# Kernel optimization log

Measured on AMD Instinct MI355X. Metric: run time of the kernel, lower is better.

Reference implementation:

```python
import jax, jax.numpy as jnp
import numpy as np

N_NODES = 50000
N_EDGES = 800000
HIDDEN = 64
RES = 0.5  # args.res_layer


def setup_inputs() -> dict:
    key = jax.random.key(0)
    ks = jax.random.split(key, 9)
    s = 0.05  # scale weights to keep exp(att) stable
    return {
        "edge_index": jax.random.randint(ks[0], (2, N_EDGES), 0, N_NODES, dtype=jnp.int32),
        "adj_values": jax.random.uniform(ks[1], (N_EDGES,), dtype=jnp.float32),
        "embeds": jax.random.normal(ks[2], (N_NODES, HIDDEN), dtype=jnp.float32),
        "W1": jax.random.normal(ks[3], (HIDDEN, HIDDEN), dtype=jnp.float32) * s,
        "b1": jax.random.normal(ks[4], (HIDDEN,), dtype=jnp.float32) * s,
        "W2": jax.random.normal(ks[5], (HIDDEN, HIDDEN), dtype=jnp.float32) * s,
        "b2": jax.random.normal(ks[6], (HIDDEN,), dtype=jnp.float32) * s,
        "att_w": jax.random.normal(ks[7], (2 * HIDDEN,), dtype=jnp.float32) * s,
        "att_b": jax.random.normal(ks[8], (1,), dtype=jnp.float32) * s,
    }


def reference(edge_index, adj_values, embeds, W1, b1, W2, b2, att_w, att_b):
    n = embeds.shape[0]
    h = embeds.shape[1]
    row, col = edge_index[0], edge_index[1]
    # per-edge gather + two small linears with ReLU
    f1 = jax.nn.relu(embeds[row] @ W1 + b1)          # [E, h]
    f2 = jax.nn.relu(embeds[col] @ W2 + b2)          # [E, h]
    # attention score = Linear(concat(f1, f2)) -> split weight, avoid concat
    att = f1 @ att_w[:h] + f2 @ att_w[h:] + att_b[0]  # [E]
    exp_att = jnp.exp(att)
    # sparse row-wise softmax denominator via segment sum
    rowsum = jax.ops.segment_sum(exp_att, row, num_segments=n) + 1e-6  # [N]
    values = (exp_att / rowsum[row] + RES * adj_values) / (1.0 + RES)  # [E]
    # SpMM: out[i] = sum_{e: row[e]=i} values[e] * embeds[col[e]]
    out = jax.ops.segment_sum(values[:, None] * embeds[col], row, num_segments=n)  # [N, h]
    return values, out
```

## Files before the change

kernel.cpp:

```cpp
#include <hip/hip_runtime.h>
#include <hip/hip_bf16.h>

#define HID 64
#define RES_F 0.5f
#define NBKT 196
#define BCAP 5120
#define EB   256
#define LCAP 48

typedef __attribute__((ext_vector_type(8))) short short8;
typedef __attribute__((ext_vector_type(4))) float f32x4;

__device__ __forceinline__ float lane_bcast_f(float v, int k) {
    return __builtin_bit_cast(float, __builtin_amdgcn_readlane(__builtin_bit_cast(int, v), k));
}
__device__ __forceinline__ short f2bf(float x) {
    __hip_bfloat16 h = __float2bfloat16(x);
    return __builtin_bit_cast(short, h);
}
__device__ __forceinline__ float bf2f(unsigned short u) {
    return __builtin_bit_cast(float, ((unsigned)u) << 16);
}

__global__ void __launch_bounds__(256) fused_prep_kernel(
    const float* __restrict__ embeds,
    const float* __restrict__ W1, const float* __restrict__ W2,
    const float* __restrict__ b1, const float* __restrict__ b2,
    const float* __restrict__ att_w, const float* __restrict__ att_b,
    const int* __restrict__ row, const int* __restrict__ col,
    const float* __restrict__ adj,
    int2* __restrict__ bstream, int* __restrict__ bcnt,
    float* __restrict__ g, float* __restrict__ corr,
    __hip_bfloat16* __restrict__ embeds_bf,
    int n, int E, int nodeBlocks)
{
    __shared__ short sW[2 * HID * HID];

    if (blockIdx.x < nodeBlocks) {
        for (int i = threadIdx.x; i < HID * HID; i += blockDim.x) {
            sW[i]             = f2bf(W1[i]);
            sW[HID * HID + i] = f2bf(W2[i]);
        }
        __syncthreads();

        const float ab = att_b[0];
        const int lane = threadIdx.x & 63;
        const int colx = lane & 15;
        const int quad = lane >> 4;

        short8 bfrag[8][2];
        float  sac[8], bc[8];
#pragma unroll
        for (int cb = 0; cb < 8; ++cb) {
            const int jp = cb * 16 + colx;
            const short* w = (jp < HID) ? (sW + jp) : (sW + HID * HID + jp - HID);
#pragma unroll
            for (int kh = 0; kh < 2; ++kh) {
                short8 f;
#pragma unroll
                for (int j = 0; j < 8; ++j) {
                    const int k = kh * 32 + quad * 8 + j;
                    f[j] = w[k * HID];
                }
                bfrag[cb][kh] = f;
            }
            sac[cb] = att_w[jp];
            bc[cb]  = (jp < HID) ? b1[jp] : b2[jp - HID];
        }

        int gwave = (blockIdx.x * blockDim.x + threadIdx.x) >> 6;
        const int nwave = (nodeBlocks * blockDim.x) >> 6;
        const int nbatch = (n + 15) >> 4;

        for (int b = gwave; b < nbatch; b += nwave) {
            const int base = b << 4;
            int mrow = base + colx;
            if (mrow >= n) mrow = n - 1;
            const float* ep = embeds + (size_t)mrow * HID;
            short8 afrag0, afrag1;
#pragma unroll
            for (int j = 0; j < 8; ++j) {
                afrag0[j] = f2bf(ep[quad * 8 + j]);
                afrag1[j] = f2bf(ep[32 + quad * 8 + j]);
            }
            {
                short8* ebf = (short8*)(embeds_bf + (size_t)mrow * HID);
                ebf[quad]     = afrag0;
                ebf[4 + quad] = afrag1;
            }

            float acc1[4] = {0.f, 0.f, 0.f, 0.f};
            float acc2[4] = {0.f, 0.f, 0.f, 0.f};
#pragma unroll
            for (int cb = 0; cb < 8; ++cb) {
                f32x4 C = {0.f, 0.f, 0.f, 0.f};
                C = __builtin_amdgcn_mfma_f32_16x16x32_bf16(afrag0, bfrag[cb][0], C, 0, 0, 0);
                C = __builtin_amdgcn_mfma_f32_16x16x32_bf16(afrag1, bfrag[cb][1], C, 0, 0, 0);
#pragma unroll
                for (int reg = 0; reg < 4; ++reg) {
                    const float v = fmaxf(C[reg] + bc[cb], 0.f) * sac[cb];
                    if (cb < 4) acc1[reg] += v; else acc2[reg] += v;
                }
            }
#pragma unroll
            for (int reg = 0; reg < 4; ++reg) {
#pragma unroll
                for (int off = 1; off < 16; off <<= 1) {
                    acc1[reg] += __shfl_xor(acc1[reg], off, 64);
                    acc2[reg] += __shfl_xor(acc2[reg], off, 64);
                }
            }
            if (colx == 0) {
#pragma unroll
                for (int reg = 0; reg < 4; ++reg) {
                    const int i = base + quad * 4 + reg;
                    if (i < n) {
                        g[i]    = __expf(acc2[reg]);
                        corr[i] = 1e-6f * __expf(-(acc1[reg] + ab));
                    }
                }
            }
        }
    } else {
        int* lcnt = (int*)sW;
        for (int k = threadIdx.x; k < NBKT; k += 256) lcnt[k] = 0;
        __syncthreads();

        const int eb = blockIdx.x - nodeBlocks;
        const int chunk = (E + EB - 1) / EB;
        const int e0 = eb * chunk;
        const int e1 = min(E, e0 + chunk);
        for (int e = e0 + (int)threadIdx.x; e < e1; e += 256) {
            const int r    = row[e];
            const int c    = col[e];
            const float aj = adj[e];
            const unsigned aq = (unsigned)(aj * 65535.0f + 0.5f);
            const int k = r >> 8;
            const int2 pl = make_int2((int)((unsigned)c | (aq << 16)),
                                      (r & 255) | (e << 8));
            const int pos = atomicAdd(&lcnt[k], 1);
            if (pos < LCAP)
                bstream[((size_t)k * EB + eb) * LCAP + pos] = pl;
        }
        __syncthreads();

        for (int k = threadIdx.x; k < NBKT; k += 256)
            bcnt[eb * NBKT + k] = min(lcnt[k], LCAP);
    }
}

__global__ void __launch_bounds__(256) regroup_kernel(
    const int2* __restrict__ bstream, const int* __restrict__ bcnt,
    int2* __restrict__ edata2, int* __restrict__ rowdir, int n)
{
    __shared__ int cnt[256], scan[256], wcur[256];
    const int k = blockIdx.x;
    const int t = threadIdx.x;
    cnt[t] = 0;
    const int myc = bcnt[t * NBKT + k];
    __syncthreads();

    const int2* src = bstream + ((size_t)k * EB + t) * LCAP;
    for (int j = 0; j < myc; ++j)
        atomicAdd(&cnt[src[j].y & 255], 1);
    __syncthreads();

    scan[t] = cnt[t];
    __syncthreads();
    for (int ofs = 1; ofs < 256; ofs <<= 1) {
        const int v = (t >= ofs) ? scan[t - ofs] : 0;
        __syncthreads();
        scan[t] += v;
        __syncthreads();
    }
    const int excl = scan[t] - cnt[t];
    wcur[t] = excl;
    const int r = k * 256 + t;
    if (r < n)
        rowdir[r] = (k * BCAP + excl) | (min(cnt[t], 64) << 20);
    __syncthreads();

    int2* dst = edata2 + (size_t)k * BCAP;
    for (int j = 0; j < myc; ++j) {
        const int2 pl = src[j];
        const int p = atomicAdd(&wcur[pl.y & 255], 1);
        dst[p] = pl;
    }
}

__global__ void __launch_bounds__(256) spmm_kernel(
    const int* __restrict__ rowdir, const int2* __restrict__ edata2,
    const __hip_bfloat16* __restrict__ embeds_bf,
    const float* __restrict__ g, const float* __restrict__ corr,
    float* __restrict__ values, float* __restrict__ out, int n)
{
    const float inv = 1.0f / (1.0f + RES_F);
    const int lane = threadIdx.x & 63;
    const int half = lane >> 5;
    const int hl   = lane & 31;
    int r = (blockIdx.x * blockDim.x + threadIdx.x) >> 6;
    const int nwave = (gridDim.x * blockDim.x) >> 6;

    for (; r < n; r += nwave) {
        const int pk    = rowdir[r];
        const int start = pk & 0xFFFFF;
        const int deg   = pk >> 20;
        const bool valid = lane < deg;
        int c = 0, e = 0;
        float gc = 0.0f, aj = 0.0f;
        if (valid) {
            const int2 ed = edata2[(size_t)start + lane];
            const unsigned pk0 = (unsigned)ed.x;
            c  = (int)(pk0 & 0xFFFFu);
            aj = (float)(pk0 >> 16) * (1.0f / 65535.0f);
            e  = (int)(((unsigned)ed.y) >> 8);
            gc = g[c];
        }
        float G = gc;
#pragma unroll
        for (int off = 1; off < 64; off <<= 1)
            G += __shfl_xor(G, off, 64);
        const float invDr = 1.0f / (G + corr[r]);
        float v = 0.0f;
        if (valid) {
            v = (gc * invDr + RES_F * aj) * inv;
            values[e] = v;
        }

        float accx = 0.0f, accy = 0.0f;
        int j = 0;
        for (; j + 8 <= deg; j += 8) {
            const int j0 = j + half,     j1 = j + 2 + half;
            const int j2 = j + 4 + half, j3 = j + 6 + half;
            const int   c0 = __shfl(c, j0, 64);
            const int   c1 = __shfl(c, j1, 64);
            const int   c2 = __shfl(c, j2, 64);
            const int   c3 = __shfl(c, j3, 64);
            const float v0 = __shfl(v, j0, 64);
            const float v1 = __shfl(v, j1, 64);
            const float v2 = __shfl(v, j2, 64);
            const float v3 = __shfl(v, j3, 64);
            const ushort2 h0 = *(const ushort2*)(embeds_bf + (size_t)c0 * HID + hl * 2);
            const ushort2 h1 = *(const ushort2*)(embeds_bf + (size_t)c1 * HID + hl * 2);
            const ushort2 h2 = *(const ushort2*)(embeds_bf + (size_t)c2 * HID + hl * 2);
            const ushort2 h3 = *(const ushort2*)(embeds_bf + (size_t)c3 * HID + hl * 2);
            accx = fmaf(v0, bf2f(h0.x), accx); accy = fmaf(v0, bf2f(h0.y), accy);
            accx = fmaf(v1, bf2f(h1.x), accx); accy = fmaf(v1, bf2f(h1.y), accy);
            accx = fmaf(v2, bf2f(h2.x), accx); accy = fmaf(v2, bf2f(h2.y), accy);
            accx = fmaf(v3, bf2f(h3.x), accx); accy = fmaf(v3, bf2f(h3.y), accy);
        }
        for (; j < deg; j += 2) {
            const int j0 = j + half;
            const int   cj = __shfl(c, j0, 64);
            const float vj = __shfl(v, j0, 64);
            const ushort2 h = *(const ushort2*)(embeds_bf + (size_t)cj * HID + hl * 2);
            accx = fmaf(vj, bf2f(h.x), accx);
            accy = fmaf(vj, bf2f(h.y), accy);
        }
        accx += __shfl_xor(accx, 32, 64);
        accy += __shfl_xor(accy, 32, 64);
        if (lane < 32) {
            float2 o; o.x = accx; o.y = accy;
            ((float2*)(out + (size_t)r * HID))[hl] = o;
        }
    }
}

extern "C" void kernel_launch(void* const* d_in, const int* in_sizes, int n_in,
                              void* d_out, int out_size, void* d_ws, size_t ws_size,
                              hipStream_t stream_)
{
    const int* edge_index = (const int*)d_in[0];
    const float* adj      = (const float*)d_in[1];
    const float* embeds   = (const float*)d_in[2];
    const float* W1       = (const float*)d_in[3];
    const float* b1       = (const float*)d_in[4];
    const float* W2       = (const float*)d_in[5];
    const float* b2       = (const float*)d_in[6];
    const float* att_w    = (const float*)d_in[7];
    const float* att_b    = (const float*)d_in[8];

    const int E = in_sizes[1];
    const int N = in_sizes[2] / HID;

    const int* row = edge_index;
    const int* col = edge_index + E;

    int2*  bstream = (int2*)d_ws;
    int2*  edata2  = bstream + (size_t)NBKT * EB * LCAP;
    int*   bcnt    = (int*)(edata2 + (size_t)NBKT * BCAP);
    int*   rowdir  = bcnt + EB * NBKT;
    float* g       = (float*)(rowdir + N);
    float* corr    = g + N;
    __hip_bfloat16* embeds_bf = (__hip_bfloat16*)(corr + N);

    float* values = (float*)d_out;
    float* out    = values + E;

    const int nodeBlocks = 512;
    fused_prep_kernel<<<nodeBlocks + EB, 256, 0, stream_>>>(
        embeds, W1, W2, b1, b2, att_w, att_b, row, col, adj,
        bstream, bcnt, g, corr, embeds_bf,
        N, E, nodeBlocks);

    regroup_kernel<<<NBKT, 256, 0, stream_>>>(bstream, bcnt, edata2, rowdir, N);

    spmm_kernel<<<12544, 256, 0, stream_>>>(rowdir, edata2, embeds_bf,
                                            g, corr, values, out, N);
}
```

Before: 144.5 us.

## Move softmax normalization into regroup and write values in a coalesced pass

The per-row denominator is now accumulated with shared-memory float atomics during regroup, and final edge values are computed there and stored in edata2 in place of the packed adj and edge id. The SpMM kernel no longer does a wave reduction, gathers g, or scatters to values[e]. A new elementwise kernel writes values coalesced in edge order using an invD array. Regroup runs 512 threads per block, splits each bucket's edges between two halves, and uses a wave-shuffle scan instead of the barrier-heavy scan. The trade-offs are an extra launch, extra g/invD gathers, and a denominator summed in atomic order.

```diff
diff --git a/kernel.cpp b/kernel.cpp
--- a/kernel.cpp
+++ b/kernel.cpp
@@ -11,9 +11,6 @@
 typedef __attribute__((ext_vector_type(8))) short short8;
 typedef __attribute__((ext_vector_type(4))) float f32x4;
 
-__device__ __forceinline__ float lane_bcast_f(float v, int k) {
-    return __builtin_bit_cast(float, __builtin_amdgcn_readlane(__builtin_bit_cast(int, v), k));
-}
 __device__ __forceinline__ short f2bf(float x) {
     __hip_bfloat16 h = __float2bfloat16(x);
     return __builtin_bit_cast(short, h);
@@ -149,52 +146,86 @@
     }
 }
 
-__global__ void __launch_bounds__(256) regroup_kernel(
+__global__ void __launch_bounds__(512) regroup_kernel(
     const int2* __restrict__ bstream, const int* __restrict__ bcnt,
-    int2* __restrict__ edata2, int* __restrict__ rowdir, int n)
-{
-    __shared__ int cnt[256], scan[256], wcur[256];
-    const int k = blockIdx.x;
-    const int t = threadIdx.x;
-    cnt[t] = 0;
-    const int myc = bcnt[t * NBKT + k];
+    const float* __restrict__ g, const float* __restrict__ corr,
+    int2* __restrict__ edata2, int* __restrict__ rowdir,
+    float* __restrict__ invD, int n)
+{
+    __shared__ int   cnt[256], wcur[256], wsum[4];
+    __shared__ float Dsum[256];
+    const int k  = blockIdx.x;
+    const int t  = threadIdx.x;
+    const int sl = t & 255;
+    const bool hi = t >= 256;
+
+    if (!hi) {
+        cnt[sl] = 0;
+        const int r = k * 256 + sl;
+        Dsum[sl] = (r < n) ? corr[r] : 1.0f;
+    }
+    const int myc = bcnt[sl * NBKT + k];
+    const int jm  = (myc + 1) >> 1;
+    const int j0  = hi ? jm : 0;
+    const int j1  = hi ? myc : jm;
     __syncthreads();
 
-    const int2* src = bstream + ((size_t)k * EB + t) * LCAP;
-    for (int j = 0; j < myc; ++j)
-        atomicAdd(&cnt[src[j].y & 255], 1);
+    const int2* src = bstream + ((size_t)k * EB + sl) * LCAP;
+    for (int j = j0; j < j1; ++j) {
+        const int2 pl = src[j];
+        const int rloc = pl.y & 255;
+        atomicAdd(&cnt[rloc], 1);
+        atomicAdd(&Dsum[rloc], g[pl.x & 0xFFFF]);
+    }
     __syncthreads();
 
-    scan[t] = cnt[t];
+    int incl = 0, myCnt = 0;
+    if (!hi) {
+        const int lane = t & 63;
+        myCnt = cnt[t];
+        incl = myCnt;
+#pragma unroll
+        for (int off = 1; off < 64; off <<= 1) {
+            const int y = __shfl_up(incl, off, 64);
+            if (lane >= off) incl += y;
+        }
+        if (lane == 63) wsum[t >> 6] = incl;
+    }
     __syncthreads();
-    for (int ofs = 1; ofs < 256; ofs <<= 1) {
-        const int v = (t >= ofs) ? scan[t - ofs] : 0;
-        __syncthreads();
-        scan[t] += v;
-        __syncthreads();
-    }
-    const int excl = scan[t] - cnt[t];
-    wcur[t] = excl;
-    const int r = k * 256 + t;
-    if (r < n)
-        rowdir[r] = (k * BCAP + excl) | (min(cnt[t], 64) << 20);
+    if (!hi) {
+        const int w = t >> 6;
+        int wo = 0;
+        for (int i = 0; i < w; ++i) wo += wsum[i];
+        const int excl = incl + wo - myCnt;
+        wcur[t] = excl;
+        const float iD = 1.0f / Dsum[t];
+        const int r = k * 256 + t;
+        if (r < n) {
+            rowdir[r] = (k * BCAP + excl) | (min(myCnt, 64) << 20);
+            invD[r]   = iD;
+        }
+        Dsum[t] = iD;
+    }
     __syncthreads();
 
+    const float inv = 1.0f / (1.0f + RES_F);
     int2* dst = edata2 + (size_t)k * BCAP;
-    for (int j = 0; j < myc; ++j) {
+    for (int j = j0; j < j1; ++j) {
         const int2 pl = src[j];
-        const int p = atomicAdd(&wcur[pl.y & 255], 1);
-        dst[p] = pl;
+        const int rloc = pl.y & 255;
+        const int c    = pl.x & 0xFFFF;
+        const float aj = (float)((unsigned)pl.x >> 16) * (1.0f / 65535.0f);
+        const float v  = (g[c] * Dsum[rloc] + RES_F * aj) * inv;
+        const int p = atomicAdd(&wcur[rloc], 1);
+        dst[p] = make_int2(c, __float_as_int(v));
     }
 }
 
 __global__ void __launch_bounds__(256) spmm_kernel(
     const int* __restrict__ rowdir, const int2* __restrict__ edata2,
     const __hip_bfloat16* __restrict__ embeds_bf,
-    const float* __restrict__ g, const float* __restrict__ corr,
-    float* __restrict__ values, float* __restrict__ out, int n)
-{
-    const float inv = 1.0f / (1.0f + RES_F);
+    float* __restrict__ out, int n)
+{
     const int lane = threadIdx.x & 63;
     const int half = lane >> 5;
     const int hl   = lane & 31;
@@ -205,26 +236,12 @@
         const int pk    = rowdir[r];
         const int start = pk & 0xFFFFF;
         const int deg   = pk >> 20;
-        const bool valid = lane < deg;
-        int c = 0, e = 0;
-        float gc = 0.0f, aj = 0.0f;
-        if (valid) {
+        int c = 0;
+        float v = 0.0f;
+        if (lane < deg) {
             const int2 ed = edata2[(size_t)start + lane];
-            const unsigned pk0 = (unsigned)ed.x;
-            c  = (int)(pk0 & 0xFFFFu);
-            aj = (float)(pk0 >> 16) * (1.0f / 65535.0f);
-            e  = (int)(((unsigned)ed.y) >> 8);
-            gc = g[c];
-        }
-        float G = gc;
-#pragma unroll
-        for (int off = 1; off < 64; off <<= 1)
-            G += __shfl_xor(G, off, 64);
-        const float invDr = 1.0f / (G + corr[r]);
-        float v = 0.0f;
-        if (valid) {
-            v = (gc * invDr + RES_F * aj) * inv;
-            values[e] = v;
+            c = ed.x;
+            v = __int_as_float(ed.y);
         }
 
         float accx = 0.0f, accy = 0.0f;
@@ -266,6 +283,19 @@
     }
 }
 
+__global__ void __launch_bounds__(256) values_kernel(
+    const int* __restrict__ row, const int* __restrict__ col,
+    const float* __restrict__ adj,
+    const float* __restrict__ g, const float* __restrict__ invD,
+    float* __restrict__ values, int E)
+{
+    const int e = blockIdx.x * blockDim.x + threadIdx.x;
+    if (e < E) {
+        const float inv = 1.0f / (1.0f + RES_F);
+        values[e] = (g[col[e]] * invD[row[e]] + RES_F * adj[e]) * inv;
+    }
+}
+
 extern "C" void kernel_launch(void* const* d_in, const int* in_sizes, int n_in,
                               void* d_out, int out_size, void* d_ws, size_t ws_size,
                               hipStream_t stream_)
@@ -292,7 +322,8 @@
     int*   rowdir  = bcnt + EB * NBKT;
     float* g       = (float*)(rowdir + N);
     float* corr    = g + N;
-    __hip_bfloat16* embeds_bf = (__hip_bfloat16*)(corr + N);
+    float* invD    = corr + N;
+    __hip_bfloat16* embeds_bf = (__hip_bfloat16*)(invD + N);
 
     float* values = (float*)d_out;
     float* out    = values + E;
@@ -303,8 +334,12 @@
         bstream, bcnt, g, corr, embeds_bf,
         N, E, nodeBlocks);
 
-    regroup_kernel<<<NBKT, 256, 0, stream_>>>(bstream, bcnt, edata2, rowdir, N);
+    regroup_kernel<<<NBKT, 512, 0, stream_>>>(bstream, bcnt, g, corr,
+                                              edata2, rowdir, invD, N);
 
     spmm_kernel<<<12544, 256, 0, stream_>>>(rowdir, edata2, embeds_bf,
-                                            g, corr, values, out, N);
-}
+                                            out, N);
+
+    values_kernel<<<(E + 255) / 256, 256, 0, stream_>>>(row, col, adj, g,
+                                                        invD, values, E);
+}
```

Measured after the change: 147.5 us. 1.02x slower.

## Split regroup across 512 threads with wave-shuffle scan and remap spmm rows to waves

Applied to the files above, without the earlier changes.

The regroup kernel now runs 512 threads per bucket, each half handling half of every bucket sub-stream. The 256-entry block scan, which needed log-many barriers, becomes a wave-level shuffle scan plus a small cross-wave sum. The spmm kernel drops its grid-stride loop and assigns one row per wave with a block index permutation, so the 8 blocks sharing an index mod 8 cover interleaved buckets. This is meant to cut serial latency in regroup and spread edata2 and rowdir accesses across buckets, at the cost of more launched blocks and some early-exiting waves.

```diff
diff --git a/kernel.cpp b/kernel.cpp
--- a/kernel.cpp
+++ b/kernel.cpp
@@ -11,9 +11,6 @@
 typedef __attribute__((ext_vector_type(8))) short short8;
 typedef __attribute__((ext_vector_type(4))) float f32x4;
 
-__device__ __forceinline__ float lane_bcast_f(float v, int k) {
-    return __builtin_bit_cast(float, __builtin_amdgcn_readlane(__builtin_bit_cast(int, v), k));
-}
 __device__ __forceinline__ short f2bf(float x) {
     __hip_bfloat16 h = __float2bfloat16(x);
     return __builtin_bit_cast(short, h);
@@ -149,39 +146,54 @@
     }
 }
 
-__global__ void __launch_bounds__(256) regroup_kernel(
+__global__ void __launch_bounds__(512) regroup_kernel(
     const int2* __restrict__ bstream, const int* __restrict__ bcnt,
     int2* __restrict__ edata2, int* __restrict__ rowdir, int n)
 {
-    __shared__ int cnt[256], scan[256], wcur[256];
-    const int k = blockIdx.x;
-    const int t = threadIdx.x;
-    cnt[t] = 0;
-    const int myc = bcnt[t * NBKT + k];
+    __shared__ int cnt[256], wcur[256], wsum[4];
+    const int k  = blockIdx.x;
+    const int t  = threadIdx.x;
+    const int sl = t & 255;
+    const bool hi = t >= 256;
+
+    if (!hi) cnt[sl] = 0;
+    const int myc = bcnt[sl * NBKT + k];
+    const int jm  = (myc + 1) >> 1;
+    const int j0  = hi ? jm : 0;
+    const int j1  = hi ? myc : jm;
     __syncthreads();
 
-    const int2* src = bstream + ((size_t)k * EB + t) * LCAP;
-    for (int j = 0; j < myc; ++j)
+    const int2* src = bstream + ((size_t)k * EB + sl) * LCAP;
+    for (int j = j0; j < j1; ++j)
         atomicAdd(&cnt[src[j].y & 255], 1);
     __syncthreads();
 
-    scan[t] = cnt[t];
+    int incl = 0, myCnt = 0;
+    if (!hi) {
+        const int lane = t & 63;
+        myCnt = cnt[t];
+        incl = myCnt;
+#pragma unroll
+        for (int off = 1; off < 64; off <<= 1) {
+            const int y = __shfl_up(incl, off, 64);
+            if (lane >= off) incl += y;
+        }
+        if (lane == 63) wsum[t >> 6] = incl;
+    }
     __syncthreads();
-    for (int ofs = 1; ofs < 256; ofs <<= 1) {
-        const int v = (t >= ofs) ? scan[t - ofs] : 0;
-        __syncthreads();
-        scan[t] += v;
-        __syncthreads();
-    }
-    const int excl = scan[t] - cnt[t];
-    wcur[t] = excl;
-    const int r = k * 256 + t;
-    if (r < n)
-        rowdir[r] = (k * BCAP + excl) | (min(cnt[t], 64) << 20);
+    if (!hi) {
+        int wo = 0;
+        for (int i = 0; i < (t >> 6); ++i) wo += wsum[i];
+        const int excl = incl + wo - myCnt;
+        wcur[t] = excl;
+        const int r = k * 256 + t;
+        if (r < n)
+            rowdir[r] = (k * BCAP + excl) | (min(myCnt, 64) << 20);
+    }
     __syncthreads();
 
     int2* dst = edata2 + (size_t)k * BCAP;
-    for (int j = 0; j < myc; ++j) {
+    for (int j = j0; j < j1; ++j) {
         const int2 pl = src[j];
         const int p = atomicAdd(&wcur[pl.y & 255], 1);
         dst[p] = pl;
@@ -198,71 +210,72 @@
     const int lane = threadIdx.x & 63;
     const int half = lane >> 5;
     const int hl   = lane & 31;
-    int r = (blockIdx.x * blockDim.x + threadIdx.x) >> 6;
-    const int nwave = (gridDim.x * blockDim.x) >> 6;
-
-    for (; r < n; r += nwave) {
-        const int pk    = rowdir[r];
-        const int start = pk & 0xFFFFF;
-        const int deg   = pk >> 20;
-        const bool valid = lane < deg;
-        int c = 0, e = 0;
-        float gc = 0.0f, aj = 0.0f;
-        if (valid) {
-            const int2 ed = edata2[(size_t)start + lane];
-            const unsigned pk0 = (unsigned)ed.x;
-            c  = (int)(pk0 & 0xFFFFu);
-            aj = (float)(pk0 >> 16) * (1.0f / 65535.0f);
-            e  = (int)(((unsigned)ed.y) >> 8);
-            gc = g[c];
-        }
-        float G = gc;
-#pragma unroll
-        for (int off = 1; off < 64; off <<= 1)
-            G += __shfl_xor(G, off, 64);
-        const float invDr = 1.0f / (G + corr[r]);
-        float v = 0.0f;
-        if (valid) {
-            v = (gc * invDr + RES_F * aj) * inv;
-            values[e] = v;
-        }
-
-        float accx = 0.0f, accy = 0.0f;
-        int j = 0;
-        for (; j + 8 <= deg; j += 8) {
-            const int j0 = j + half,     j1 = j + 2 + half;
-            const int j2 = j + 4 + half, j3 = j + 6 + half;
-            const int   c0 = __shfl(c, j0, 64);
-            const int   c1 = __shfl(c, j1, 64);
-            const int   c2 = __shfl(c, j2, 64);
-            const int   c3 = __shfl(c, j3, 64);
-            const float v0 = __shfl(v, j0, 64);
-            const float v1 = __shfl(v, j1, 64);
-            const float v2 = __shfl(v, j2, 64);
-            const float v3 = __shfl(v, j3, 64);
-            const ushort2 h0 = *(const ushort2*)(embeds_bf + (size_t)c0 * HID + hl * 2);
-            const ushort2 h1 = *(const ushort2*)(embeds_bf + (size_t)c1 * HID + hl * 2);
-            const ushort2 h2 = *(const ushort2*)(embeds_bf + (size_t)c2 * HID + hl * 2);
-            const ushort2 h3 = *(const ushort2*)(embeds_bf + (size_t)c3 * HID + hl * 2);
-            accx = fmaf(v0, bf2f(h0.x), accx); accy = fmaf(v0, bf2f(h0.y), accy);
-            accx = fmaf(v1, bf2f(h1.x), accx); accy = fmaf(v1, bf2f(h1.y), accy);
-            accx = fmaf(v2, bf2f(h2.x), accx); accy = fmaf(v2, bf2f(h2.y), accy);
-            accx = fmaf(v3, bf2f(h3.x), accx); accy = fmaf(v3, bf2f(h3.y), accy);
-        }
-        for (; j < deg; j += 2) {
-            const int j0 = j + half;
-            const int   cj = __shfl(c, j0, 64);
-            const float vj = __shfl(v, j0, 64);
-            const ushort2 h = *(const ushort2*)(embeds_bf + (size_t)cj * HID + hl * 2);
-            accx = fmaf(vj, bf2f(h.x), accx);
-            accy = fmaf(vj, bf2f(h.y), accy);
-        }
-        accx += __shfl_xor(accx, 32, 64);
-        accy += __shfl_xor(accy, 32, 64);
-        if (lane < 32) {
-            float2 o; o.x = accx; o.y = accy;
-            ((float2*)(out + (size_t)r * HID))[hl] = o;
-        }
+
+    const int idx = ((blockIdx.x >> 3) << 2) + (threadIdx.x >> 6);
+    const int k   = ((idx >> 8) << 3) + (blockIdx.x & 7);
+    const int r   = (k << 8) + (idx & 255);
+    if (k >= NBKT || r >= n) return;
+
+    const int pk    = rowdir[r];
+    const int start = pk & 0xFFFFF;
+    const int deg   = pk >> 20;
+    const bool valid = lane < deg;
+    int c = 0, e = 0;
+    float gc = 0.0f, aj = 0.0f;
+    if (valid) {
+        const int2 ed = edata2[(size_t)start + lane];
+        const unsigned pk0 = (unsigned)ed.x;
+        c  = (int)(pk0 & 0xFFFFu);
+        aj = (float)(pk0 >> 16) * (1.0f / 65535.0f);
+        e  = (int)(((unsigned)ed.y) >> 8);
+        gc = g[c];
+    }
+    float G = gc;
+#pragma unroll
+    for (int off = 1; off < 64; off <<= 1)
+        G += __shfl_xor(G, off, 64);
+    const float invDr = 1.0f / (G + corr[r]);
+    float v = 0.0f;
+    if (valid) {
+        v = (gc * invDr + RES_F * aj) * inv;
+        values[e] = v;
+    }
+
+    float accx = 0.0f, accy = 0.0f;
+    int j = 0;
+    for (; j + 8 <= deg; j += 8) {
+        const int j0 = j + half,     j1 = j + 2 + half;
+        const int j2 = j + 4 + half, j3 = j + 6 + half;
+        const int   c0 = __shfl(c, j0, 64);
+        const int   c1 = __shfl(c, j1, 64);
+        const int   c2 = __shfl(c, j2, 64);
+        const int   c3 = __shfl(c, j3, 64);
+        const float v0 = __shfl(v, j0, 64);
+        const float v1 = __shfl(v, j1, 64);
+        const float v2 = __shfl(v, j2, 64);
+        const float v3 = __shfl(v, j3, 64);
+        const ushort2 h0 = *(const ushort2*)(embeds_bf + (size_t)c0 * HID + hl * 2);
+        const ushort2 h1 = *(const ushort2*)(embeds_bf + (size_t)c1 * HID + hl * 2);
+        const ushort2 h2 = *(const ushort2*)(embeds_bf + (size_t)c2 * HID + hl * 2);
+        const ushort2 h3 = *(const ushort2*)(embeds_bf + (size_t)c3 * HID + hl * 2);
+        accx = fmaf(v0, bf2f(h0.x), accx); accy = fmaf(v0, bf2f(h0.y), accy);
+        accx = fmaf(v1, bf2f(h1.x), accx); accy = fmaf(v1, bf2f(h1.y), accy);
+        accx = fmaf(v2, bf2f(h2.x), accx); accy = fmaf(v2, bf2f(h2.y), accy);
+        accx = fmaf(v3, bf2f(h3.x), accx); accy = fmaf(v3, bf2f(h3.y), accy);
+    }
+    for (; j < deg; j += 2) {
+        const int j0 = j + half;
+        const int   cj = __shfl(c, j0, 64);
+        const float vj = __shfl(v, j0, 64);
+        const ushort2 h = *(const ushort2*)(embeds_bf + (size_t)cj * HID + hl * 2);
+        accx = fmaf(vj, bf2f(h.x), accx);
+        accy = fmaf(vj, bf2f(h.y), accy);
+    }
+    accx += __shfl_xor(accx, 32, 64);
+    accy += __shfl_xor(accy, 32, 64);
+    if (lane < 32) {
+        float2 o; o.x = accx; o.y = accy;
+        ((float2*)(out + (size_t)r * HID))[hl] = o;
     }
 }
 
@@ -303,8 +316,8 @@
         bstream, bcnt, g, corr, embeds_bf,
         N, E, nodeBlocks);
 
-    regroup_kernel<<<NBKT, 256, 0, stream_>>>(bstream, bcnt, edata2, rowdir, N);
-
-    spmm_kernel<<<12544, 256, 0, stream_>>>(rowdir, edata2, embeds_bf,
+    regroup_kernel<<<NBKT, 512, 0, stream_>>>(bstream, bcnt, edata2, rowdir, N);
+
+    spmm_kernel<<<12800, 256, 0, stream_>>>(rowdir, edata2, embeds_bf,
                                             g, corr, values, out, N);
 }
```

After: 144.4 us. No clear change (-0.0%).
